# Optimization experiments

Hardware: AMD Instinct MI355X
Metric: run time of the kernel (lower is better)

Reference implementation:

```python
import jax, jax.numpy as jnp
import numpy as np

B, C, H, W = 4, 256, 64, 64
C8 = C // 8
MH, MW = 256, 256  # mask input resolution


def _conv(x, w, b, pad, dil=1):
    out = jax.lax.conv_general_dilated(
        x, w, window_strides=(1, 1),
        padding=[(pad, pad), (pad, pad)],
        rhs_dilation=(dil, dil),
        dimension_numbers=("NCHW", "OIHW", "NCHW"))
    return out + b[None, :, None, None]


def setup_inputs() -> dict:
    key = jax.random.key(0)
    ks = jax.random.split(key, 16)

    def w_init(k, shape):
        fan_in = shape[1] * shape[2] * shape[3]
        bound = 1.0 / np.sqrt(fan_in)
        return jax.random.uniform(k, shape, jnp.float32, -bound, bound)

    def b_init(k, n, fan_in):
        bound = 1.0 / np.sqrt(fan_in)
        return jax.random.uniform(k, (n,), jnp.float32, -bound, bound)

    return {
        "x": jax.random.normal(ks[0], (B, C, H, W), jnp.float32),
        "mask": jax.random.uniform(ks[1], (B, 1, MH, MW), jnp.float32),
        "w_ctx": w_init(ks[2], (C, C, 7, 7)),   "b_ctx": b_init(ks[3], C, C * 49),
        "w_wide": w_init(ks[4], (C, C, 5, 5)),  "b_wide": b_init(ks[5], C, C * 25),
        "w_comb": w_init(ks[6], (C, 2 * C, 1, 1)), "b_comb": b_init(ks[7], C, 2 * C),
        "w_q": w_init(ks[8], (C8, C, 1, 1)),    "b_q": b_init(ks[9], C8, C),
        "w_k": w_init(ks[10], (C8, C, 1, 1)),   "b_k": b_init(ks[11], C8, C),
        "w_v": w_init(ks[12], (C, C, 1, 1)),    "b_v": b_init(ks[13], C, C),
    }


def reference(x, mask, w_ctx, b_ctx, w_wide, b_wide, w_comb, b_comb,
              w_q, b_q, w_k, b_k, w_v, b_v):
    local_ctx = _conv(x, w_ctx, b_ctx, pad=3, dil=1)          # [B,C,H,W]
    wide_ctx = _conv(x, w_wide, b_wide, pad=6, dil=3)         # [B,C,H,W]
    multi = _conv(jnp.concatenate([local_ctx, wide_ctx], axis=1),
                  w_comb, b_comb, pad=0)                       # [B,C,H,W]

    b, c, h, w = multi.shape
    n = h * w
    q = _conv(multi, w_q, b_q, pad=0).reshape(b, C8, n)        # [B,C/8,N]
    k = _conv(multi, w_k, b_k, pad=0).reshape(b, C8, n)        # [B,C/8,N]
    v = _conv(multi, w_v, b_v, pad=0).reshape(b, c, n)         # [B,C,N]

    scores = jnp.einsum("bcm,bcn->bmn", q, k)                  # [B,N,N]
    attn = jax.nn.softmax(scores, axis=-1)
    out = jnp.einsum("bcn,bmn->bcm", v, attn).reshape(b, c, h, w)

    # nearest-neighbor resize of mask to (h, w), matching torch F.interpolate
    mh, mw = mask.shape[2], mask.shape[3]
    idx_h = (jnp.arange(h) * mh) // h
    idx_w = (jnp.arange(w) * mw) // w
    mask_r = mask[:, :, idx_h][:, :, :, idx_w]                 # [B,1,h,w]

    return out * (1.0 + mask_r)
```

## Files before the change

### kernel.cpp

```cpp
#include <hip/hip_runtime.h>
#include <math.h>

#define BB 4
#define CC 256
#define HH 64
#define WW 64
#define NN 4096

typedef _Float16 f16x8 __attribute__((ext_vector_type(8)));
typedef float f32x4 __attribute__((ext_vector_type(4)));

__device__ __forceinline__ void prep_pad(
    int blk, const float* __restrict__ x, _Float16* __restrict__ xpad)
{
  int pr = blk % 76;
  int b  = blk / 76;
  int ci = threadIdx.x;
  int r = pr - 6;
  _Float16* dst = xpad + (((size_t)b*76 + pr)*76)*256 + ci;
  if (r < 0 || r >= HH) {
    for (int pc = 0; pc < 76; ++pc) dst[(size_t)pc*256] = (_Float16)0.f;
  } else {
    #pragma unroll
    for (int pc = 0; pc < 6; ++pc) dst[(size_t)pc*256] = (_Float16)0.f;
    #pragma unroll
    for (int pc = 70; pc < 76; ++pc) dst[(size_t)pc*256] = (_Float16)0.f;
    const f32x4* s4 = (const f32x4*)(x + ((size_t)b*CC + ci)*NN + (size_t)r*WW);
    for (int q = 0; q < 16; ++q) {
      f32x4 v = s4[q];
      #pragma unroll
      for (int j = 0; j < 4; ++j)
        dst[(size_t)(6 + q*4 + j)*256] = (_Float16)v[j];
    }
  }
}

__device__ __forceinline__ void prep_wcvt(
    int co, const float* __restrict__ src, _Float16* __restrict__ dst, int T)
{
  int ci = threadIdx.x;
  const float* s = src + ((size_t)co*256 + ci)*T;
  for (int t = 0; t < T; ++t)
    dst[(size_t)t*65536 + co*256 + ci] = (_Float16)s[t];
}

__device__ __forceinline__ void prep_fcvt(
    int blk, const float* __restrict__ src, _Float16* __restrict__ dst, int n)
{
  int i = blk * 256 + threadIdx.x;
  if (i < n) dst[i] = (_Float16)src[i];
}

__global__ __launch_bounds__(256) void prep_kernel(
    const float* __restrict__ x,
    const float* __restrict__ w_ctx, const float* __restrict__ w_wide,
    const float* __restrict__ w_comb, const float* __restrict__ w_q,
    const float* __restrict__ w_k, const float* __restrict__ w_v,
    _Float16* __restrict__ xpad, _Float16* __restrict__ wb7,
    _Float16* __restrict__ wb5, _Float16* __restrict__ wcombH,
    _Float16* __restrict__ wqkH, _Float16* __restrict__ wvH)
{
  int blk = blockIdx.x;
  if      (blk < 304)  prep_pad(blk, x, xpad);
  else if (blk < 560)  prep_wcvt(blk - 304, w_ctx, wb7, 49);
  else if (blk < 816)  prep_wcvt(blk - 560, w_wide, wb5, 25);
  else if (blk < 1328) prep_fcvt(blk - 816, w_comb, wcombH, 131072);
  else if (blk < 1360) prep_fcvt(blk - 1328, w_q, wqkH, 8192);
  else if (blk < 1392) prep_fcvt(blk - 1360, w_k, wqkH + 8192, 8192);
  else                 prep_fcvt(blk - 1392, w_v, wvH, 65536);
}

__global__ __launch_bounds__(64) void wfuse_kernel(
    const _Float16* __restrict__ wb7, const _Float16* __restrict__ wb5,
    const _Float16* __restrict__ wcombH,
    _Float16* __restrict__ wf7, _Float16* __restrict__ wf5)
{
  int t = blockIdx.x;
  int ct = blockIdx.y;
  int lane = threadIdx.x;
  int l15 = lane & 15, lg = lane >> 4;
  const _Float16* wb; _Float16* wf; int part;
  if (t < 49) { wb = wb7 + (size_t)t*65536; wf = wf7 + (size_t)t*65536; part = 0; }
  else        { wb = wb5 + (size_t)(t-49)*65536; wf = wf5 + (size_t)(t-49)*65536; part = 1; }
  int co0 = ct*64;
  for (int cit = 0; cit < 4; ++cit) {
    int ci0 = cit*64;
    f32x4 acc[4][4] = {};
    for (int k0 = 0; k0 < 256; k0 += 32) {
      f16x8 a[4], bfr[4];
      #pragma unroll
      for (int f = 0; f < 4; ++f)
        a[f] = *(const f16x8*)(wcombH + (size_t)(co0 + f*16 + l15)*512 + part*256 + k0 + lg*8);
      #pragma unroll
      for (int f = 0; f < 4; ++f)
        #pragma unroll
        for (int j = 0; j < 8; ++j)
          bfr[f][j] = wb[(size_t)(k0 + lg*8 + j)*256 + ci0 + f*16 + l15];
      #pragma unroll
      for (int i = 0; i < 4; ++i)
        #pragma unroll
        for (int j = 0; j < 4; ++j)
          acc[i][j] = __builtin_amdgcn_mfma_f32_16x16x32_f16(a[i], bfr[j], acc[i][j], 0, 0, 0);
    }
    #pragma unroll
    for (int i = 0; i < 4; ++i)
      #pragma unroll
      for (int j = 0; j < 4; ++j)
        #pragma unroll
        for (int r = 0; r < 4; ++r)
          wf[(size_t)(co0 + i*16 + lg*4 + r)*256 + ci0 + j*16 + l15] = (_Float16)acc[i][j][r];
  }
}

__global__ __launch_bounds__(256) void mbias_kernel(
    const float* __restrict__ w_comb, const float* __restrict__ b_comb,
    const float* __restrict__ b_ctx, const float* __restrict__ b_wide,
    float* __restrict__ mbias)
{
  int o = threadIdx.x;
  float s = b_comb[o];
  const float* wr = w_comb + (size_t)o*512;
  for (int m = 0; m < 256; ++m) s = fmaf(wr[m], b_ctx[m], s);
  for (int m = 0; m < 256; ++m) s = fmaf(wr[256 + m], b_wide[m], s);
  mbias[o] = s;
}

template<int KS, int DIL, bool BIAS>
__device__ __forceinline__ void conv_body(
    int ytile, int cot, int b,
    const _Float16* __restrict__ xpad, const _Float16* __restrict__ wb,
    const float* __restrict__ bias, _Float16* __restrict__ outp,
    char* xs)
{
  int y0 = ytile * 2;
  int tid = threadIdx.x;
  int lane = tid & 63;
  int wv = tid >> 6;
  int wco = wv >> 1;
  int wsp = wv & 1;
  int l15 = lane & 15;
  int lg  = lane >> 4;

  f32x4 acc[2][4];
  #pragma unroll
  for (int m = 0; m < 2; ++m)
    #pragma unroll
    for (int n = 0; n < 4; ++n) acc[m][n] = (f32x4){0.f, 0.f, 0.f, 0.f};

  for (int kh = 0; kh < KS; ++kh) {
    int prow = 6 + y0 + (kh - KS/2) * DIL;
    const uint4* src = (const uint4*)(xpad + (((size_t)b*76 + prow)*76)*256);
    __syncthreads();
    #pragma unroll
    for (int i = 0; i < 10; ++i) {
      int ch = tid + i*512;
      if (ch < 4864) {
        uint4 v = src[ch];
        int r = ch >> 5, cq = ch & 31;
        *(uint4*)(xs + r*512 + ((cq << 4) ^ ((r & 7) << 4))) = v;
      }
    }
    __syncthreads();
    for (int kw = 0; kw < KS; ++kw) {
      int dx = (kw - KS/2) * DIL;
      int tap = kh*KS + kw;
      const _Float16* wt = wb + ((size_t)tap << 16)
                              + ((size_t)(cot*128 + wco*32 + l15) << 8) + (lg << 3);
      #pragma unroll
      for (int half = 0; half < 2; ++half) {
        f16x8 w0[4], w1[4];
        #pragma unroll
        for (int kq = 0; kq < 4; ++kq) {
          int ks = half*4 + kq;
          w0[kq] = *(const f16x8*)(wt + ks*32);
          w1[kq] = *(const f16x8*)(wt + 16*256 + ks*32);
        }
        #pragma unroll
        for (int kq = 0; kq < 4; ++kq) {
          int ks = half*4 + kq;
          #pragma unroll
          for (int nf = 0; nf < 4; ++nf) {
            int r = wsp*76 + 6 + nf*16 + l15 + dx;
            f16x8 bf = *(const f16x8*)(xs + r*512 + ((ks*64 + (lg << 4)) ^ ((r & 7) << 4)));
            acc[0][nf] = __builtin_amdgcn_mfma_f32_16x16x32_f16(w0[kq], bf, acc[0][nf], 0, 0, 0);
            acc[1][nf] = __builtin_amdgcn_mfma_f32_16x16x32_f16(w1[kq], bf, acc[1][nf], 0, 0, 0);
          }
        }
      }
    }
  }

  __syncthreads();
  _Float16* ep = (_Float16*)xs;
  #pragma unroll
  for (int m = 0; m < 2; ++m)
    #pragma unroll
    for (int i = 0; i < 4; ++i) {
      int co_l = wco*32 + m*16 + lg*4 + i;
      float bs = BIAS ? bias[cot*128 + co_l] : 0.f;
      #pragma unroll
      for (int nf = 0; nf < 4; ++nf) {
        int n_l = wsp*64 + nf*16 + l15;
        ep[n_l*136 + co_l] = (_Float16)(acc[m][nf][i] + bs);
      }
    }
  __syncthreads();
  const int cbase = cot*128;
  #pragma unroll
  for (int it = 0; it < 4; ++it) {
    int idx = tid + it*512;
    int n_l = idx >> 4, q = idx & 15;
    f16x8 val = *(const f16x8*)(ep + n_l*136 + q*8);
    *(f16x8*)(outp + ((size_t)b*4096 + (size_t)y0*64 + n_l)*256 + cbase + q*8) = val;
  }
}

__global__ __launch_bounds__(512, 4) void conv_both_kernel(
    const _Float16* __restrict__ xpad,
    const _Float16* __restrict__ wf7, const _Float16* __restrict__ wf5,
    const float* __restrict__ mbias,
    _Float16* __restrict__ m7, _Float16* __restrict__ m5)
{
  __shared__ __align__(16) char xs[2*76*512];
  int hw = blockIdx.x;
  int k = hw & 7, s = hw >> 3;
  if (s < 32)
    conv_body<7, 1, true >(s, k >> 2, k & 3, xpad, wf7, mbias, m7, xs);
  else
    conv_body<5, 3, false>(s - 32, k & 1, k >> 1, xpad, wf5, mbias, m5, xs);
}

__global__ __launch_bounds__(64) void gemm_qk_kernel(
    const _Float16* __restrict__ A, const _Float16* __restrict__ A2,
    const _Float16* __restrict__ Wt,
    const float* __restrict__ bias0, const float* __restrict__ bias1,
    _Float16* __restrict__ outh)
{
  int nt = blockIdx.x;
  int lane = threadIdx.x;
  int l15 = lane & 15, lg = lane >> 4;
  int n0 = nt*16;
  f32x4 acc[4] = {};
  for (int k0 = 0; k0 < 256; k0 += 32) {
    size_t aoff = (size_t)(n0 + l15)*256 + k0 + lg*8;
    f16x8 a = *(const f16x8*)(A + aoff) + *(const f16x8*)(A2 + aoff);
    f16x8 bfr[4];
    #pragma unroll
    for (int f = 0; f < 4; ++f)
      bfr[f] = *(const f16x8*)(Wt + (size_t)(f*16 + l15)*256 + k0 + lg*8);
    #pragma unroll
    for (int j = 0; j < 4; ++j)
      acc[j] = __builtin_amdgcn_mfma_f32_16x16x32_f16(a, bfr[j], acc[j], 0, 0, 0);
  }
  #pragma unroll
  for (int j = 0; j < 4; ++j)
    #pragma unroll
    for (int r = 0; r < 4; ++r) {
      int n = n0 + lg*4 + r;
      int o = j*16 + l15;
      float bs = (o < 32) ? bias0[o] : bias1[o - 32];
      outh[(size_t)n*64 + o] = (_Float16)(acc[j][r] + bs);
    }
}

__global__ __launch_bounds__(64) void gemm_v_kernel(
    const _Float16* __restrict__ M, const _Float16* __restrict__ M2,
    const _Float16* __restrict__ Wv,
    const float* __restrict__ bias, _Float16* __restrict__ v)
{
  int nt = blockIdx.x;
  int ct = blockIdx.y;
  int lane = threadIdx.x;
  int l15 = lane & 15, lg = lane >> 4;
  int n0 = nt*32, c0 = ct*64;
  f32x4 acc[4][2] = {};
  for (int k0 = 0; k0 < 256; k0 += 32) {
    f16x8 a[4], bfr[2];
    #pragma unroll
    for (int f = 0; f < 4; ++f)
      a[f] = *(const f16x8*)(Wv + (size_t)(c0 + f*16 + l15)*256 + k0 + lg*8);
    #pragma unroll
    for (int f = 0; f < 2; ++f) {
      size_t moff = (size_t)(n0 + f*16 + l15)*256 + k0 + lg*8;
      bfr[f] = *(const f16x8*)(M + moff) + *(const f16x8*)(M2 + moff);
    }
    #pragma unroll
    for (int i = 0; i < 4; ++i)
      #pragma unroll
      for (int j = 0; j < 2; ++j)
        acc[i][j] = __builtin_amdgcn_mfma_f32_16x16x32_f16(a[i], bfr[j], acc[i][j], 0, 0, 0);
  }
  #pragma unroll
  for (int i = 0; i < 4; ++i)
    #pragma unroll
    for (int j = 0; j < 2; ++j)
      #pragma unroll
      for (int r = 0; r < 4; ++r) {
        int c = c0 + i*16 + lg*4 + r;
        int n_abs = n0 + j*16 + l15;
        int b = n_abs >> 12, n = n_abs & 4095;
        v[((size_t)(b*256 + c))*4096 + n] = (_Float16)(acc[i][j][r] + bias[c]);
      }
}

__global__ __launch_bounds__(256) void attn_stats_kernel(
    const _Float16* __restrict__ qh,
    float* __restrict__ rowmaxP, float* __restrict__ rowsumP)
{
  int blk = blockIdx.x;
  int b = blk >> 7, mt = (blk >> 1) & 63, nh = blk & 1;
  int tid = threadIdx.x, lane = tid & 63, w = tid >> 6;
  int l15 = lane & 15, lg = lane >> 4;
  size_t bN = (size_t)b * 4096;
  int mrow = mt*64 + w*16;
  f16x8 ah = *(const f16x8*)(qh + (bN + mrow + l15)*64 + lg*8);
  float rm[4] = {-3e38f, -3e38f, -3e38f, -3e38f};
  float sm[4] = {0.f, 0.f, 0.f, 0.f};
  for (int n0 = nh*2048; n0 < nh*2048 + 2048; n0 += 16) {
    f16x8 bh = *(const f16x8*)(qh + (bN + n0 + l15)*64 + 32 + lg*8);
    f32x4 s = {};
    s = __builtin_amdgcn_mfma_f32_16x16x32_f16(ah, bh, s, 0, 0, 0);
    #pragma unroll
    for (int i = 0; i < 4; ++i) {
      float nm = fmaxf(rm[i], s[i]);
      sm[i] = sm[i]*__expf(rm[i] - nm) + __expf(s[i] - nm);
      rm[i] = nm;
    }
  }
  #pragma unroll
  for (int off = 1; off <= 8; off <<= 1) {
    #pragma unroll
    for (int i = 0; i < 4; ++i) {
      float rmo = __shfl_xor(rm[i], off);
      float smo = __shfl_xor(sm[i], off);
      float M = fmaxf(rm[i], rmo);
      sm[i] = sm[i]*__expf(rm[i] - M) + smo*__expf(rmo - M);
      rm[i] = M;
    }
  }
  if (l15 == 0) {
    #pragma unroll
    for (int i = 0; i < 4; ++i) {
      size_t idx = (size_t)nh*16384 + bN + mrow + lg*4 + i;
      rowmaxP[idx] = rm[i];
      rowsumP[idx] = sm[i];
    }
  }
}

__global__ __launch_bounds__(512) void attn_out_kernel(
    const _Float16* __restrict__ qh, const _Float16* __restrict__ v,
    const float* __restrict__ rowmaxP, const float* __restrict__ rowsumP,
    const float* __restrict__ mask, float* __restrict__ out)
{
  __shared__ union U {
    struct { __align__(16) _Float16 vs[256*40]; __align__(16) _Float16 pl[64*40]; } s;
    float epi[256*68];
  } u;
  int blk = blockIdx.x;
  int b = blk >> 6, mt = blk & 63;
  int tid = threadIdx.x, lane = tid & 63, w = tid >> 6;
  int l15 = lane & 15, lg = lane >> 4;
  size_t bN = (size_t)b * 4096;
  int m0 = mt*64;

  int mf = w >> 1, nf2 = w & 1;
  f16x8 ah = *(const f16x8*)(qh + (bN + m0 + mf*16 + l15)*64 + lg*8);
  float rm[4], rsi[4];
  #pragma unroll
  for (int i = 0; i < 4; ++i) {
    size_t m = bN + m0 + mf*16 + lg*4 + i;
    float r0 = rowmaxP[m], r1 = rowmaxP[16384 + m];
    float s0 = rowsumP[m], s1 = rowsumP[16384 + m];
    float M = fmaxf(r0, r1);
    rm[i] = M;
    rsi[i] = 1.0f / (s0*__expf(r0 - M) + s1*__expf(r1 - M));
  }
  int mh = w >> 2, cw = (w & 3)*64;
  f32x4 acc[2][4] = {};
  const _Float16* vb = v + (size_t)b*256*4096;

  for (int n0 = 0; n0 < 4096; n0 += 32) {
    #pragma unroll
    for (int it = 0; it < 2; ++it) {
      int idx = tid + it*512;
      int c = idx >> 2, q = idx & 3;
      *(f16x8*)(u.s.vs + c*40 + q*8) = *(const f16x8*)(vb + (size_t)c*4096 + n0 + q*8);
    }
    {
      f16x8 bh = *(const f16x8*)(qh + (bN + n0 + nf2*16 + l15)*64 + 32 + lg*8);
      f32x4 s = {};
      s = __builtin_amdgcn_mfma_f32_16x16x32_f16(ah, bh, s, 0, 0, 0);
      #pragma unroll
      for (int i = 0; i < 4; ++i) {
        float p = __expf(s[i] - rm[i]) * rsi[i];
        u.s.pl[(mf*16 + lg*4 + i)*40 + nf2*16 + l15] = (_Float16)p;
      }
    }
    __syncthreads();
    {
      f16x8 pa[2], pb[4];
      #pragma unroll
      for (int af = 0; af < 2; ++af)
        pa[af] = *(const f16x8*)(u.s.pl + (mh*32 + af*16 + l15)*40 + lg*8);
      #pragma unroll
      for (int bf = 0; bf < 4; ++bf)
        pb[bf] = *(const f16x8*)(u.s.vs + (cw + bf*16 + l15)*40 + lg*8);
      #pragma unroll
      for (int af = 0; af < 2; ++af)
        #pragma unroll
        for (int bf = 0; bf < 4; ++bf)
          acc[af][bf] = __builtin_amdgcn_mfma_f32_16x16x32_f16(pa[af], pb[bf], acc[af][bf], 0, 0, 0);
    }
    __syncthreads();
  }

  #pragma unroll
  for (int af = 0; af < 2; ++af)
    #pragma unroll
    for (int bf = 0; bf < 4; ++bf)
      #pragma unroll
      for (int r = 0; r < 4; ++r) {
        int c = cw + bf*16 + l15;
        int ml = mh*32 + af*16 + lg*4 + r;
        u.epi[c*68 + ml] = acc[af][bf][r];
      }
  __syncthreads();
  const float* mb = mask + (size_t)b*65536 + (size_t)(mt*4)*256;
  #pragma unroll
  for (int it = 0; it < 8; ++it) {
    int idx = tid + it*512;
    int c = idx >> 4, q = idx & 15;
    f32x4 val = *(const f32x4*)(u.epi + c*68 + q*4);
    f32x4 o4;
    #pragma unroll
    for (int jj = 0; jj < 4; ++jj) {
      int xcol = q*4 + jj;
      o4[jj] = val[jj] * (1.0f + mb[xcol*4]);
    }
    *(f32x4*)(out + ((size_t)b*256 + c)*4096 + m0 + q*4) = o4;
  }
}

extern "C" void kernel_launch(void* const* d_in, const int* in_sizes, int n_in,
                              void* d_out, int out_size, void* d_ws, size_t ws_size,
                              hipStream_t stream)
{
  (void)in_sizes; (void)n_in; (void)out_size; (void)ws_size;
  const float* x      = (const float*)d_in[0];
  const float* mask   = (const float*)d_in[1];
  const float* w_ctx  = (const float*)d_in[2];
  const float* b_ctx  = (const float*)d_in[3];
  const float* w_wide = (const float*)d_in[4];
  const float* b_wide = (const float*)d_in[5];
  const float* w_comb = (const float*)d_in[6];
  const float* b_comb = (const float*)d_in[7];
  const float* w_q    = (const float*)d_in[8];
  const float* b_q    = (const float*)d_in[9];
  const float* w_k    = (const float*)d_in[10];
  const float* b_k    = (const float*)d_in[11];
  const float* w_v    = (const float*)d_in[12];
  const float* b_v    = (const float*)d_in[13];
  float* out = (float*)d_out;

  float* ws = (float*)d_ws;
  _Float16* xpad    = (_Float16*)(ws);
  _Float16* wb7     = (_Float16*)(ws + 2957312);
  _Float16* wb5     = (_Float16*)(ws + 4562944);
  _Float16* wcombH  = (_Float16*)(ws + 5382144);
  _Float16* wqkH    = (_Float16*)(ws + 5447680);
  _Float16* wvH     = (_Float16*)(ws + 5455872);
  _Float16* wf7     = (_Float16*)(ws + 5488640);
  _Float16* wf5     = (_Float16*)(ws + 7094272);
  float*    mbias   = ws + 7913472;
  _Float16* m7      = (_Float16*)(ws + 7913728);
  _Float16* m5      = (_Float16*)(ws + 10010880);
  _Float16* qkt_h   = (_Float16*)(ws);
  float*    rowmaxP = ws + 524288;
  float*    rowsumP = ws + 557056;
  _Float16* vbuf    = (_Float16*)(ws + 589824);

  prep_kernel<<<1648, 256, 0, stream>>>(x, w_ctx, w_wide, w_comb, w_q, w_k,
                                        w_v, xpad, wb7, wb5, wcombH, wqkH, wvH);
  wfuse_kernel<<<dim3(74, 4), 64, 0, stream>>>(wb7, wb5, wcombH, wf7, wf5);
  mbias_kernel<<<1, 256, 0, stream>>>(w_comb, b_comb, b_ctx, b_wide, mbias);

  conv_both_kernel<<<512, 512, 0, stream>>>(xpad, wf7, wf5, mbias, m7, m5);

  gemm_qk_kernel<<<1024, 64, 0, stream>>>(m7, m5, wqkH, b_q, b_k, qkt_h);
  gemm_v_kernel<<<dim3(512, 4), 64, 0, stream>>>(m7, m5, wvH, b_v, vbuf);

  attn_stats_kernel<<<512, 256, 0, stream>>>(qkt_h, rowmaxP, rowsumP);
  attn_out_kernel<<<256, 512, 0, stream>>>(qkt_h, vbuf, rowmaxP, rowsumP,
                                           mask, out);
}
```

Measured before the change: 529.4 us.

## Compute all output channels per conv block with larger per-wave register tile

Each conv block now produces all 256 output channels for its two-row spatial tile instead of 128. Each wave holds a 64×64 accumulator tile (4×4 MFMA fragments) rather than 32×64. This halves the grid and halves how often the padded input rows are staged into LDS per output, and each B fragment read from LDS now feeds four MFMAs instead of two. The cost is twice the accumulator registers, launch bounds lowered to 2 blocks per CU, and only 256 blocks, which may leave the 7x7 and 5x5 work unevenly balanced across CUs.

```diff
diff --git a/kernel.cpp b/kernel.cpp
--- a/kernel.cpp
+++ b/kernel.cpp
@@ -127,7 +127,7 @@
 
 template<int KS, int DIL, bool BIAS>
 __device__ __forceinline__ void conv_body(
-    int ytile, int cot, int b,
+    int ytile, int b,
     const _Float16* __restrict__ xpad, const _Float16* __restrict__ wb,
     const float* __restrict__ bias, _Float16* __restrict__ outp,
     char* xs)
@@ -136,16 +136,16 @@
   int tid = threadIdx.x;
   int lane = tid & 63;
   int wv = tid >> 6;
-  int wco = wv >> 1;
+  int cs  = wv >> 1;
   int wsp = wv & 1;
   int l15 = lane & 15;
   int lg  = lane >> 4;
 
-  f32x4 acc[2][4];
-  #pragma unroll
-  for (int m = 0; m < 2; ++m)
-    #pragma unroll
-    for (int n = 0; n < 4; ++n) acc[m][n] = (f32x4){0.f, 0.f, 0.f, 0.f};
+  f32x4 acc[4][4];
+  #pragma unroll
+  for (int i = 0; i < 4; ++i)
+    #pragma unroll
+    for (int j = 0; j < 4; ++j) acc[i][j] = (f32x4){0.f, 0.f, 0.f, 0.f};
 
   for (int kh = 0; kh < KS; ++kh) {
     int prow = 6 + y0 + (kh - KS/2) * DIL;
@@ -165,27 +165,23 @@
       int dx = (kw - KS/2) * DIL;
       int tap = kh*KS + kw;
       const _Float16* wt = wb + ((size_t)tap << 16)
-                              + ((size_t)(cot*128 + wco*32 + l15) << 8) + (lg << 3);
-      #pragma unroll
-      for (int half = 0; half < 2; ++half) {
-        f16x8 w0[4], w1[4];
-        #pragma unroll
-        for (int kq = 0; kq < 4; ++kq) {
-          int ks = half*4 + kq;
-          w0[kq] = *(const f16x8*)(wt + ks*32);
-          w1[kq] = *(const f16x8*)(wt + 16*256 + ks*32);
+                              + ((size_t)(cs*64 + l15) << 8) + (lg << 3);
+      #pragma unroll
+      for (int ks = 0; ks < 8; ++ks) {
+        f16x8 w[4], bf[4];
+        #pragma unroll
+        for (int jA = 0; jA < 4; ++jA)
+          w[jA] = *(const f16x8*)(wt + (size_t)jA*16*256 + ks*32);
+        #pragma unroll
+        for (int nf = 0; nf < 4; ++nf) {
+          int r = wsp*76 + 6 + nf*16 + l15 + dx;
+          bf[nf] = *(const f16x8*)(xs + r*512 + ((ks*64 + (lg << 4)) ^ ((r & 7) << 4)));
         }
         #pragma unroll
-        for (int kq = 0; kq < 4; ++kq) {
-          int ks = half*4 + kq;
+        for (int jA = 0; jA < 4; ++jA)
           #pragma unroll
-          for (int nf = 0; nf < 4; ++nf) {
-            int r = wsp*76 + 6 + nf*16 + l15 + dx;
-            f16x8 bf = *(const f16x8*)(xs + r*512 + ((ks*64 + (lg << 4)) ^ ((r & 7) << 4)));
-            acc[0][nf] = __builtin_amdgcn_mfma_f32_16x16x32_f16(w0[kq], bf, acc[0][nf], 0, 0, 0);
-            acc[1][nf] = __builtin_amdgcn_mfma_f32_16x16x32_f16(w1[kq], bf, acc[1][nf], 0, 0, 0);
-          }
-        }
+          for (int nf = 0; nf < 4; ++nf)
+            acc[jA][nf] = __builtin_amdgcn_mfma_f32_16x16x32_f16(w[jA], bf[nf], acc[jA][nf], 0, 0, 0);
       }
     }
   }
@@ -193,41 +189,39 @@
   __syncthreads();
   _Float16* ep = (_Float16*)xs;
   #pragma unroll
-  for (int m = 0; m < 2; ++m)
-    #pragma unroll
-    for (int i = 0; i < 4; ++i) {
-      int co_l = wco*32 + m*16 + lg*4 + i;
-      float bs = BIAS ? bias[cot*128 + co_l] : 0.f;
+  for (int jA = 0; jA < 4; ++jA)
+    #pragma unroll
+    for (int r = 0; r < 4; ++r) {
+      int co_l = cs*64 + jA*16 + lg*4 + r;
+      float bs = BIAS ? bias[co_l] : 0.f;
       #pragma unroll
       for (int nf = 0; nf < 4; ++nf) {
         int n_l = wsp*64 + nf*16 + l15;
-        ep[n_l*136 + co_l] = (_Float16)(acc[m][nf][i] + bs);
+        ep[n_l*264 + co_l] = (_Float16)(acc[jA][nf][r] + bs);
       }
     }
   __syncthreads();
-  const int cbase = cot*128;
-  #pragma unroll
-  for (int it = 0; it < 4; ++it) {
+  #pragma unroll
+  for (int it = 0; it < 8; ++it) {
     int idx = tid + it*512;
-    int n_l = idx >> 4, q = idx & 15;
-    f16x8 val = *(const f16x8*)(ep + n_l*136 + q*8);
-    *(f16x8*)(outp + ((size_t)b*4096 + (size_t)y0*64 + n_l)*256 + cbase + q*8) = val;
-  }
-}
-
-__global__ __launch_bounds__(512, 4) void conv_both_kernel(
+    int n_l = idx >> 5, q = idx & 31;
+    f16x8 val = *(const f16x8*)(ep + n_l*264 + q*8);
+    *(f16x8*)(outp + ((size_t)b*4096 + (size_t)y0*64 + n_l)*256 + q*8) = val;
+  }
+}
+
+__global__ __launch_bounds__(512, 2) void conv_both_kernel(
     const _Float16* __restrict__ xpad,
     const _Float16* __restrict__ wf7, const _Float16* __restrict__ wf5,
     const float* __restrict__ mbias,
     _Float16* __restrict__ m7, _Float16* __restrict__ m5)
 {
   __shared__ __align__(16) char xs[2*76*512];
-  int hw = blockIdx.x;
-  int k = hw & 7, s = hw >> 3;
-  if (s < 32)
-    conv_body<7, 1, true >(s, k >> 2, k & 3, xpad, wf7, mbias, m7, xs);
+  int blk = blockIdx.x;
+  if (blk < 128)
+    conv_body<7, 1, true >(blk & 31, blk >> 5, xpad, wf7, mbias, m7, xs);
   else
-    conv_body<5, 3, false>(s - 32, k & 1, k >> 1, xpad, wf5, mbias, m5, xs);
+    conv_body<5, 3, false>(blk & 31, (blk - 128) >> 5, xpad, wf5, mbias, m5, xs);
 }
 
 __global__ __launch_bounds__(64) void gemm_qk_kernel(
@@ -485,7 +479,7 @@
   wfuse_kernel<<<dim3(74, 4), 64, 0, stream>>>(wb7, wb5, wcombH, wf7, wf5);
   mbias_kernel<<<1, 256, 0, stream>>>(w_comb, b_comb, b_ctx, b_wide, mbias);
 
-  conv_both_kernel<<<512, 512, 0, stream>>>(xpad, wf7, wf5, mbias, m7, m5);
+  conv_both_kernel<<<256, 512, 0, stream>>>(xpad, wf7, wf5, mbias, m7, m5);
 
   gemm_qk_kernel<<<1024, 64, 0, stream>>>(m7, m5, wqkH, b_q, b_k, qkt_h);
   gemm_v_kernel<<<dim3(512, 4), 64, 0, stream>>>(m7, m5, wvH, b_v, vbuf);
```

Result: slower. 609.8 us (+15.2%).
